# Kernel tuning notes

Hardware: AMD Instinct MI355X
Metric: run time of the kernel (lower is better)

The kernel has to match this reference:

```python
import jax, jax.numpy as jnp
import numpy as np

N = 50000   # nodes
E = 800000  # edges
IN, HID, OUT = 128, 128, 64


def setup_inputs() -> dict:
    key = jax.random.key(0)
    ks = jax.random.split(key, 16)
    x = jax.random.normal(ks[0], (N, IN), dtype=jnp.float32)
    src = jax.random.randint(ks[1], (E,), 0, N, dtype=jnp.int32)
    dst = jax.random.randint(ks[2], (E,), 0, N, dtype=jnp.int32)
    s = 1.0 / np.sqrt(IN)
    W_self1 = jax.random.normal(ks[3], (IN, HID), dtype=jnp.float32) * s
    W_neigh1 = jax.random.normal(ks[4], (IN, HID), dtype=jnp.float32) * s
    b1 = jnp.zeros((HID,), dtype=jnp.float32)
    W_self2 = jax.random.normal(ks[5], (HID, HID), dtype=jnp.float32) * s
    W_neigh2 = jax.random.normal(ks[6], (HID, HID), dtype=jnp.float32) * s
    b2 = jnp.zeros((HID,), dtype=jnp.float32)
    W_self3 = jax.random.normal(ks[7], (HID, OUT), dtype=jnp.float32) * s
    W_neigh3 = jax.random.normal(ks[8], (HID, OUT), dtype=jnp.float32) * s
    b3 = jnp.zeros((OUT,), dtype=jnp.float32)
    # dropout(p=0.5) masks, pre-scaled by 1/(1-p)
    keep = 0.5
    mask1 = (jax.random.uniform(ks[9], (N, HID)) < keep).astype(jnp.float32) / keep
    mask2 = (jax.random.uniform(ks[10], (N, HID)) < keep).astype(jnp.float32) / keep
    return dict(x=x, src=src, dst=dst,
                W_self1=W_self1, W_neigh1=W_neigh1, b1=b1,
                W_self2=W_self2, W_neigh2=W_neigh2, b2=b2,
                W_self3=W_self3, W_neigh3=W_neigh3, b3=b3,
                mask1=mask1, mask2=mask2)


def _mean_agg(h, src, dst):
    # gather source features, segment-sum into destinations, divide by in-degree
    summed = jax.ops.segment_sum(h[src], dst, num_segments=N)  # [N, d]
    deg = jax.ops.segment_sum(jnp.ones((E,), dtype=h.dtype), dst, num_segments=N)
    return summed / jnp.maximum(deg, 1.0)[:, None]


def _sage_layer(h, src, dst, W_self, W_neigh, b):
    h_neigh = _mean_agg(h, src, dst)
    return h @ W_self + h_neigh @ W_neigh + b


def reference(x, src, dst, W_self1, W_neigh1, b1, W_self2, W_neigh2, b2,
              W_self3, W_neigh3, b3, mask1, mask2):
    h = _sage_layer(x, src, dst, W_self1, W_neigh1, b1)
    h = jax.nn.relu(h) * mask1
    h = _sage_layer(h, src, dst, W_self2, W_neigh2, b2)
    h = jax.nn.relu(h) * mask2
    h = _sage_layer(h, src, dst, W_self3, W_neigh3, b3)
    return h
```

## Files before the change

### kernel.cpp

```cpp
#include <hip/hip_runtime.h>
#include <hip/hip_bf16.h>

#define DIN  128
#define DHID 128
#define DOUT 64

#define EB   4096
#define CAPB 5120

typedef short short8 __attribute__((ext_vector_type(8)));
typedef float f32x4  __attribute__((ext_vector_type(4)));

__device__ __forceinline__ ushort f2bf(float f) {
    union { float f; uint u; } c; c.f = f;
    uint u = c.u;
    return (ushort)((u + 0x7fff + ((u >> 16) & 1)) >> 16);
}
__device__ __forceinline__ float bf2f(uint h16) {
    union { uint u; float f; } c; c.u = h16 << 16;
    return c.f;
}
__device__ __forceinline__ float sb8(uint u, int k) {
    return (float)((int)(u << (24 - 8 * k)) >> 24);
}

__device__ __forceinline__ void wprep_dev(const float* __restrict__ W,
                                          ushort* __restrict__ Wt, int OUT, int idx) {
    int nn = idx >> 7;
    int k  = idx & 127;
    Wt[idx] = f2bf(W[(size_t)k * OUT + nn]);
}

__global__ __launch_bounds__(256)
void megaprep(const int* __restrict__ src, const int* __restrict__ dst, int E, int fillB,
              int* __restrict__ bkt_cur, uint* __restrict__ pairs,
              const float* __restrict__ x, ushort* __restrict__ xb, int n4, int cvtB,
              const float* __restrict__ Ws1, const float* __restrict__ Wn1,
              const float* __restrict__ Ws2, const float* __restrict__ Wn2,
              const float* __restrict__ Ws3, const float* __restrict__ Wn3,
              ushort* __restrict__ Wst1, ushort* __restrict__ Wnt1,
              ushort* __restrict__ Wst2, ushort* __restrict__ Wnt2,
              ushort* __restrict__ Wst3, ushort* __restrict__ Wnt3) {
    __shared__ int c[256];
    __shared__ int startl[256];
    __shared__ int ofs[256];
    int b = blockIdx.x;
    const int t = threadIdx.x;
    if (b < fillB) {
        c[t] = 0;
        __syncthreads();
        const int base = b * EB;
        const int end = min(base + EB, E);
        for (int i = base + t; i < end; i += 256)
            atomicAdd(&c[dst[i] >> 8], 1);
        __syncthreads();
        int v = c[t];
        startl[t] = v ? (t * CAPB + atomicAdd(&bkt_cur[t], v)) : 0;
        ofs[t] = 0;
        __syncthreads();
        for (int i = base + t; i < end; i += 256) {
            int d = dst[i];
            int bb = d >> 8;
            int p = startl[bb] + atomicAdd(&ofs[bb], 1);
            pairs[p] = ((uint)src[i] << 8) | (uint)(d & 255);
        }
        return;
    }
    b -= fillB;
    if (b < cvtB) {
        int i = b * 256 + t;
        if (i < n4) {
            float4 v = ((const float4*)x)[i];
            ushort4 o;
            o.x = f2bf(v.x); o.y = f2bf(v.y); o.z = f2bf(v.z); o.w = f2bf(v.w);
            ((ushort4*)xb)[i] = o;
        }
        return;
    }
    b -= cvtB;
    if (b < 64)  { wprep_dev(Ws1, Wst1, 128, b * 256 + t); return; }
    b -= 64;
    if (b < 64)  { wprep_dev(Wn1, Wnt1, 128, b * 256 + t); return; }
    b -= 64;
    if (b < 64)  { wprep_dev(Ws2, Wst2, 128, b * 256 + t); return; }
    b -= 64;
    if (b < 64)  { wprep_dev(Wn2, Wnt2, 128, b * 256 + t); return; }
    b -= 64;
    if (b < 32)  { wprep_dev(Ws3, Wst3, 64, b * 256 + t); return; }
    b -= 32;
    wprep_dev(Wn3, Wnt3, 64, b * 256 + t);
}

__global__ __launch_bounds__(256)
void bucket_csr(const uint* __restrict__ pairs, const int* __restrict__ bkt_cur,
                int* __restrict__ row_ptr, int* __restrict__ deg,
                int* __restrict__ esrc, int N, int nbkt) {
    constexpr int CAP = 6144;
    __shared__ uint pl[CAP];
    __shared__ int cnt[256];
    __shared__ int rs[256];
    __shared__ int sc[256];
    const int bkt = blockIdx.x;
    const int t = threadIdx.x;
    const int ebase = bkt * CAPB;
    const int ecnt  = min(bkt_cur[bkt], CAPB);
    cnt[t] = 0;
    __syncthreads();
    const bool fits = (ecnt <= CAP);
    if (fits) {
        for (int i = t; i < ecnt; i += 256) {
            uint p = pairs[ebase + i];
            pl[i] = p;
            atomicAdd(&cnt[p & 255u], 1);
        }
    } else {
        for (int i = t; i < ecnt; i += 256)
            atomicAdd(&cnt[pairs[ebase + i] & 255u], 1);
    }
    __syncthreads();
    int own = cnt[t];
    sc[t] = own;
    __syncthreads();
    for (int o = 1; o < 256; o <<= 1) {
        int u = (t >= o) ? sc[t - o] : 0;
        __syncthreads();
        sc[t] += u;
        __syncthreads();
    }
    rs[t] = sc[t] - own;
    const int node = bkt * 256 + t;
    if (node < N) {
        row_ptr[node] = ebase + rs[t];
        deg[node] = own;
    }
    __syncthreads();
    if (fits) {
        for (int i = t; i < ecnt; i += 256) {
            uint p = pl[i];
            int pos = atomicAdd(&rs[p & 255u], 1);
            esrc[ebase + pos] = (int)(p >> 8);
        }
    } else {
        for (int i = t; i < ecnt; i += 256) {
            uint p = pairs[ebase + i];
            int pos = atomicAdd(&rs[p & 255u], 1);
            esrc[ebase + pos] = (int)(p >> 8);
        }
    }
}

template<int OUTW>
__global__ __launch_bounds__(256)
void sage_gemm(const ushort* __restrict__ Hb,
               const ushort* __restrict__ Wst,
               const ushort* __restrict__ Wnt,
               ushort* __restrict__ S,
               signed char* __restrict__ Gq,
               float* __restrict__ Gsc,
               int n) {
    constexpr int NT = OUTW / 16;
    __shared__ ushort Wl[2][OUTW * 128];

    const int tid  = threadIdx.x;
    const int lane = tid & 63;
    const int wave = tid >> 6;
    const int rg   = wave >> 1;
    const int isG  = wave & 1;
    const int m16  = lane & 15;
    const int kb   = lane >> 4;
    const int rbase = blockIdx.x * 64 + rg * 32;

    {
        const uint4* s4 = (const uint4*)Wst;
        const uint4* n4 = (const uint4*)Wnt;
        uint4* ls = (uint4*)&Wl[0][0];
        uint4* ln = (uint4*)&Wl[1][0];
#pragma unroll
        for (int j = tid; j < OUTW * 128 / 8; j += 256) {
            ls[j] = s4[j];
            ln[j] = n4[j];
        }
    }

    short8 a[2][4];
#pragma unroll
    for (int mt = 0; mt < 2; ++mt) {
        int arow = rbase + mt * 16 + m16;
        if (arow >= n) arow = n - 1;
        const ushort* __restrict__ Ap = &Hb[(size_t)arow * 128 + kb * 8];
#pragma unroll
        for (int c = 0; c < 4; ++c)
            a[mt][c] = *(const short8*)(Ap + c * 32);
    }

    __syncthreads();

    f32x4 acc[2][NT];
#pragma unroll
    for (int mt = 0; mt < 2; ++mt)
#pragma unroll
        for (int t = 0; t < NT; ++t) acc[mt][t] = (f32x4)(0.f);

    const ushort* __restrict__ Wp = &Wl[isG][0];
#pragma unroll
    for (int t = 0; t < NT; ++t) {
#pragma unroll
        for (int c = 0; c < 4; ++c) {
            short8 b = *(const short8*)&Wp[(t * 16 + m16) * 128 + c * 32 + kb * 8];
            acc[0][t] = __builtin_amdgcn_mfma_f32_16x16x32_bf16(a[0][c], b, acc[0][t], 0, 0, 0);
            acc[1][t] = __builtin_amdgcn_mfma_f32_16x16x32_bf16(a[1][c], b, acc[1][t], 0, 0, 0);
        }
    }

#pragma unroll
    for (int mt = 0; mt < 2; ++mt) {
        const int rb = rbase + mt * 16;
        if (!isG) {
#pragma unroll
            for (int r = 0; r < 4; ++r) {
                int row = rb + kb * 4 + r;
                if (row >= n) continue;
#pragma unroll
                for (int t = 0; t < NT; ++t)
                    S[(size_t)row * OUTW + t * 16 + m16] = f2bf(acc[mt][t][r]);
            }
        } else {
#pragma unroll
            for (int r = 0; r < 4; ++r) {
                float mx = 0.f;
#pragma unroll
                for (int t = 0; t < NT; ++t) mx = fmaxf(mx, fabsf(acc[mt][t][r]));
                mx = fmaxf(mx, __shfl_xor(mx, 1));
                mx = fmaxf(mx, __shfl_xor(mx, 2));
                mx = fmaxf(mx, __shfl_xor(mx, 4));
                mx = fmaxf(mx, __shfl_xor(mx, 8));
                int row = rb + kb * 4 + r;
                if (row >= n) continue;
                float inv = (mx > 0.f) ? 127.f / mx : 0.f;
                if (m16 == 0) Gsc[row] = mx * (1.f / 127.f);
#pragma unroll
                for (int t = 0; t < NT; ++t) {
                    int q = (int)rintf(acc[mt][t][r] * inv);
                    q = max(-127, min(127, q));
                    Gq[(size_t)row * OUTW + t * 16 + m16] = (signed char)q;
                }
            }
        }
    }
}

__device__ __forceinline__ void acc8(float* af, uint2 v, float sc) {
    af[0] += sc * sb8(v.x, 0); af[1] += sc * sb8(v.x, 1);
    af[2] += sc * sb8(v.x, 2); af[3] += sc * sb8(v.x, 3);
    af[4] += sc * sb8(v.y, 0); af[5] += sc * sb8(v.y, 1);
    af[6] += sc * sb8(v.y, 2); af[7] += sc * sb8(v.y, 3);
}
__device__ __forceinline__ void acc16(float* af, uint4 v, float sc) {
    af[0]  += sc * sb8(v.x, 0); af[1]  += sc * sb8(v.x, 1);
    af[2]  += sc * sb8(v.x, 2); af[3]  += sc * sb8(v.x, 3);
    af[4]  += sc * sb8(v.y, 0); af[5]  += sc * sb8(v.y, 1);
    af[6]  += sc * sb8(v.y, 2); af[7]  += sc * sb8(v.y, 3);
    af[8]  += sc * sb8(v.z, 0); af[9]  += sc * sb8(v.z, 1);
    af[10] += sc * sb8(v.z, 2); af[11] += sc * sb8(v.z, 3);
    af[12] += sc * sb8(v.w, 0); af[13] += sc * sb8(v.w, 1);
    af[14] += sc * sb8(v.w, 2); af[15] += sc * sb8(v.w, 3);
}

#define SPAN_CAP 1024

template<bool FINAL>
__global__ __launch_bounds__(256)
void sage_gather(const signed char* __restrict__ Gq, const float* __restrict__ Gsc,
                 const ushort* __restrict__ S, const float* __restrict__ bias,
                 const float* __restrict__ mask,
                 const int* __restrict__ row_ptr, const int* __restrict__ deg,
                 const int* __restrict__ esrc,
                 void* __restrict__ outv, int n) {
    __shared__ int   idx_s[SPAN_CAP];
    __shared__ float sc_s[SPAN_CAP];

    const int tid  = threadIdx.x;
    const int lane = tid & 63;
    const int wave = tid >> 6;
    const int g    = lane >> 3;
    const int l8   = lane & 7;
    const int base = blockIdx.x * 32;

    const int last   = min(base + 31, n - 1);
    const int span_s = row_ptr[base];
    const int span_e = row_ptr[last] + deg[last];
    const int len    = span_e - span_s;
    const bool staged = (len <= SPAN_CAP);
    if (staged) {
        int sA[4];
#pragma unroll
        for (int r = 0; r < 4; ++r) {
            int i = tid + r * 256;
            sA[r] = (i < len) ? esrc[span_s + i] : 0;
        }
#pragma unroll
        for (int r = 0; r < 4; ++r) {
            int i = tid + r * 256;
            if (i < len) { idx_s[i] = sA[r]; sc_s[i] = Gsc[sA[r]]; }
        }
    }
    __syncthreads();

    const int node = base + wave * 8 + g;
    if (node >= n) return;
    const int d = deg[node];
    const float inv = 1.f / fmaxf((float)d, 1.f);

    if (!FINAL) {
        float af[16];
#pragma unroll
        for (int q = 0; q < 16; ++q) af[q] = 0.f;
        const signed char* __restrict__ gp = Gq + l8 * 16;
        if (staged) {
            int i = row_ptr[node] - span_s, e = i + d;
            for (; i + 7 < e; i += 8) {
                uint4 v[8]; float c[8];
#pragma unroll
                for (int k = 0; k < 8; ++k) {
                    int ns = idx_s[i + k];
                    v[k] = *(const uint4*)&gp[(size_t)ns * 128];
                    c[k] = sc_s[i + k];
                }
#pragma unroll
                for (int k = 0; k < 8; ++k) acc16(af, v[k], c[k]);
            }
            for (; i < e; ++i) {
                int ns = idx_s[i];
                acc16(af, *(const uint4*)&gp[(size_t)ns * 128], sc_s[i]);
            }
        } else {
            int i = row_ptr[node], e = i + d;
            for (; i < e; ++i) {
                int ns = esrc[i];
                acc16(af, *(const uint4*)&gp[(size_t)ns * 128], Gsc[ns]);
            }
        }
        const int col0 = l8 * 16;
        uint4 sa = *(const uint4*)&S[(size_t)node * 128 + col0];
        uint4 sb = *(const uint4*)&S[(size_t)node * 128 + col0 + 8];
        float bv[16], mv[16];
#pragma unroll
        for (int q = 0; q < 4; ++q) {
            *(float4*)&bv[q * 4] = *(const float4*)&bias[col0 + q * 4];
            *(float4*)&mv[q * 4] = *(const float4*)&mask[(size_t)node * 128 + col0 + q * 4];
        }
        uint sv[8] = {sa.x, sa.y, sa.z, sa.w, sb.x, sb.y, sb.z, sb.w};
        uint pk[8];
#pragma unroll
        for (int q = 0; q < 8; ++q) {
            float z0 = bf2f(sv[q] & 0xffffu) + af[2 * q]     * inv + bv[2 * q];
            float z1 = bf2f(sv[q] >> 16)     + af[2 * q + 1] * inv + bv[2 * q + 1];
            z0 = fmaxf(z0, 0.f) * mv[2 * q];
            z1 = fmaxf(z1, 0.f) * mv[2 * q + 1];
            pk[q] = (uint)f2bf(z0) | ((uint)f2bf(z1) << 16);
        }
        ushort* op = (ushort*)outv + (size_t)node * 128 + col0;
        uint4 o0, o1;
        o0.x = pk[0]; o0.y = pk[1]; o0.z = pk[2]; o0.w = pk[3];
        o1.x = pk[4]; o1.y = pk[5]; o1.z = pk[6]; o1.w = pk[7];
        *(uint4*)op = o0;
        *(uint4*)(op + 8) = o1;
    } else {
        float af[8];
#pragma unroll
        for (int q = 0; q < 8; ++q) af[q] = 0.f;
        const signed char* __restrict__ gp = Gq + l8 * 8;
        if (staged) {
            int i = row_ptr[node] - span_s, e = i + d;
            for (; i + 7 < e; i += 8) {
                uint2 v[8]; float c[8];
#pragma unroll
                for (int k = 0; k < 8; ++k) {
                    int ns = idx_s[i + k];
                    v[k] = *(const uint2*)&gp[(size_t)ns * 64];
                    c[k] = sc_s[i + k];
                }
#pragma unroll
                for (int k = 0; k < 8; ++k) acc8(af, v[k], c[k]);
            }
            for (; i < e; ++i) {
                int ns = idx_s[i];
                acc8(af, *(const uint2*)&gp[(size_t)ns * 64], sc_s[i]);
            }
        } else {
            int i = row_ptr[node], e = i + d;
            for (; i < e; ++i) {
                int ns = esrc[i];
                acc8(af, *(const uint2*)&gp[(size_t)ns * 64], Gsc[ns]);
            }
        }
        const int col0 = l8 * 8;
        uint4 sv4 = *(const uint4*)&S[(size_t)node * 64 + col0];
        float bv[8];
        *(float4*)&bv[0] = *(const float4*)&bias[col0];
        *(float4*)&bv[4] = *(const float4*)&bias[col0 + 4];
        uint sv[4] = {sv4.x, sv4.y, sv4.z, sv4.w};
        float z[8];
#pragma unroll
        for (int q = 0; q < 4; ++q) {
            z[2 * q]     = bf2f(sv[q] & 0xffffu) + af[2 * q]     * inv + bv[2 * q];
            z[2 * q + 1] = bf2f(sv[q] >> 16)     + af[2 * q + 1] * inv + bv[2 * q + 1];
        }
        float* op = (float*)outv + (size_t)node * 64 + col0;
        float4 o0, o1;
        o0.x = z[0]; o0.y = z[1]; o0.z = z[2]; o0.w = z[3];
        o1.x = z[4]; o1.y = z[5]; o1.z = z[6]; o1.w = z[7];
        *(float4*)&op[0] = o0;
        *(float4*)&op[4] = o1;
    }
}

extern "C" void kernel_launch(void* const* d_in, const int* in_sizes, int n_in,
                              void* d_out, int out_size, void* d_ws, size_t ws_size,
                              hipStream_t stream) {
    const float* x   = (const float*)d_in[0];
    const int*   src = (const int*)d_in[1];
    const int*   dst = (const int*)d_in[2];
    const float* Ws1 = (const float*)d_in[3];
    const float* Wn1 = (const float*)d_in[4];
    const float* b1  = (const float*)d_in[5];
    const float* Ws2 = (const float*)d_in[6];
    const float* Wn2 = (const float*)d_in[7];
    const float* b2  = (const float*)d_in[8];
    const float* Ws3 = (const float*)d_in[9];
    const float* Wn3 = (const float*)d_in[10];
    const float* b3  = (const float*)d_in[11];
    const float* mask1 = (const float*)d_in[12];
    const float* mask2 = (const float*)d_in[13];
    float* out = (float*)d_out;

    const int N = in_sizes[0] / DIN;
    const int E = in_sizes[1];
    const int nbkt = (N + 255) >> 8;

    char* ws = (char*)d_ws;
    int* bkt_cur  = (int*)ws;
    int* row_ptr  = bkt_cur + 256;
    int* deg      = row_ptr + N;
    int* esrc     = deg + N;
    size_t off = ((size_t)(256 + 2 * N + nbkt * CAPB) * sizeof(int) + 255) & ~(size_t)255;
    uint* pairs  = (uint*)(ws + off);    off += (size_t)nbkt * CAPB * 4;
    ushort* xb   = (ushort*)(ws + off);  off += (size_t)N * 128 * 2;
    ushort* h1b  = (ushort*)(ws + off);  off += (size_t)N * 128 * 2;
    ushort* h2b  = (ushort*)(ws + off);  off += (size_t)N * 128 * 2;
    ushort* S    = (ushort*)(ws + off);  off += (size_t)N * 128 * 2;
    signed char* Gq = (signed char*)(ws + off); off += (size_t)N * 128;
    float* Gsc   = (float*)(ws + off);   off += (size_t)N * 4;
    ushort* Wst1 = (ushort*)(ws + off);  off += 128 * 128 * 2;
    ushort* Wnt1 = (ushort*)(ws + off);  off += 128 * 128 * 2;
    ushort* Wst2 = (ushort*)(ws + off);  off += 128 * 128 * 2;
    ushort* Wnt2 = (ushort*)(ws + off);  off += 128 * 128 * 2;
    ushort* Wst3 = (ushort*)(ws + off);  off += 64 * 128 * 2;
    ushort* Wnt3 = (ushort*)(ws + off);  off += 64 * 128 * 2;

    const int n4 = N * 128 / 4;
    const int cvtB = (n4 + 255) / 256;
    const int fillB = (E + EB - 1) / EB;

    hipMemsetAsync(bkt_cur, 0, 256 * sizeof(int), stream);
    megaprep<<<fillB + cvtB + 4 * 64 + 2 * 32, 256, 0, stream>>>(
        src, dst, E, fillB, bkt_cur, pairs,
        x, xb, n4, cvtB,
        Ws1, Wn1, Ws2, Wn2, Ws3, Wn3,
        Wst1, Wnt1, Wst2, Wnt2, Wst3, Wnt3);

    bucket_csr<<<nbkt, 256, 0, stream>>>(pairs, bkt_cur, row_ptr, deg, esrc, N, nbkt);

    const int gemmB = (N + 63) / 64;
    const int gathB = (N + 31) / 32;

    sage_gemm<128><<<gemmB, 256, 0, stream>>>(xb, Wst1, Wnt1, S, Gq, Gsc, N);
    sage_gather<false><<<gathB, 256, 0, stream>>>(Gq, Gsc, S, b1, mask1, row_ptr, deg, esrc, h1b, N);
    sage_gemm<128><<<gemmB, 256, 0, stream>>>(h1b, Wst2, Wnt2, S, Gq, Gsc, N);
    sage_gather<false><<<gathB, 256, 0, stream>>>(Gq, Gsc, S, b2, mask2, row_ptr, deg, esrc, h2b, N);
    sage_gemm<64><<<gemmB, 256, 0, stream>>>(h2b, Wst3, Wnt3, S, Gq, Gsc, N);
    sage_gather<true><<<gathB, 256, 0, stream>>>(Gq, Gsc, S, b3, nullptr, row_ptr, deg, esrc, out, N);
}
```

Before: 291.3 us.

## Stage gather indices per wave and double-buffer neighbor loads in sage_gather

Each wave now stages the edge span for its own 8 nodes into a private LDS slice. Source index and scale are packed together as a uint2, so the block-wide __syncthreads and the two separate LDS arrays go away. Blocks shrink to 128 threads, and the fixed 8-wide gather loop becomes a two-buffer software pipeline of 4-edge groups, so the next group's loads are issued while the current one accumulates. The aim is to remove block-level sync stalls and overlap gather latency with compute. In exchange it adds more code paths and relies on in-wave LDS ordering without an explicit barrier.

New measurement: 284.3 us. -2.4%, faster.

```diff
diff --git a/kernel.cpp b/kernel.cpp
--- a/kernel.cpp
+++ b/kernel.cpp
@@ -266,49 +266,71 @@
     af[14] += sc * sb8(v.w, 2); af[15] += sc * sb8(v.w, 3);
 }
 
-#define SPAN_CAP 1024
+#define WCAP 320
+
+#define LOADW16(V, C, base_)                                        \
+    _Pragma("unroll")                                               \
+    for (int k = 0; k < 4; ++k) {                                   \
+        uint2 p = iw[(base_) + k];                                  \
+        V[k] = *(const uint4*)&gp[(size_t)p.x * 128];               \
+        C[k] = __uint_as_float(p.y);                                \
+    }
+#define LOADW8(V, C, base_)                                         \
+    _Pragma("unroll")                                               \
+    for (int k = 0; k < 4; ++k) {                                   \
+        uint2 p = iw[(base_) + k];                                  \
+        V[k] = *(const uint2*)&gp[(size_t)p.x * 64];                \
+        C[k] = __uint_as_float(p.y);                                \
+    }
+#define CONSW16(V, C)                                               \
+    _Pragma("unroll") for (int k = 0; k < 4; ++k) acc16(af, V[k], C[k]);
+#define CONSW8(V, C)                                                \
+    _Pragma("unroll") for (int k = 0; k < 4; ++k) acc8(af, V[k], C[k]);
 
 template<bool FINAL>
-__global__ __launch_bounds__(256)
+__global__ __launch_bounds__(128)
 void sage_gather(const signed char* __restrict__ Gq, const float* __restrict__ Gsc,
                  const ushort* __restrict__ S, const float* __restrict__ bias,
                  const float* __restrict__ mask,
                  const int* __restrict__ row_ptr, const int* __restrict__ deg,
                  const int* __restrict__ esrc,
                  void* __restrict__ outv, int n) {
-    __shared__ int   idx_s[SPAN_CAP];
-    __shared__ float sc_s[SPAN_CAP];
+    __shared__ uint2 is_s[2][WCAP];
 
     const int tid  = threadIdx.x;
+    const int wave = tid >> 6;
     const int lane = tid & 63;
-    const int wave = tid >> 6;
     const int g    = lane >> 3;
     const int l8   = lane & 7;
-    const int base = blockIdx.x * 32;
-
-    const int last   = min(base + 31, n - 1);
-    const int span_s = row_ptr[base];
+    const int wbase = blockIdx.x * 16 + wave * 8;
+    if (wbase >= n) return;
+
+    const int node = wbase + g;
+    int d = 0, rp = 0;
+    if (node < n) { d = deg[node]; rp = row_ptr[node]; }
+
+    const int last   = min(wbase + 7, n - 1);
+    const int span_s = row_ptr[wbase];
     const int span_e = row_ptr[last] + deg[last];
     const int len    = span_e - span_s;
-    const bool staged = (len <= SPAN_CAP);
+    uint2* __restrict__ iw = is_s[wave];
+    const bool staged = (len <= WCAP);
     if (staged) {
-        int sA[4];
-#pragma unroll
-        for (int r = 0; r < 4; ++r) {
-            int i = tid + r * 256;
+        int sA[5];
+#pragma unroll
+        for (int r = 0; r < 5; ++r) {
+            int i = lane + r * 64;
             sA[r] = (i < len) ? esrc[span_s + i] : 0;
         }
 #pragma unroll
-        for (int r = 0; r < 4; ++r) {
-            int i = tid + r * 256;
-            if (i < len) { idx_s[i] = sA[r]; sc_s[i] = Gsc[sA[r]]; }
-        }
-    }
-    __syncthreads();
-
-    const int node = base + wave * 8 + g;
+        for (int r = 0; r < 5; ++r) {
+            int i = lane + r * 64;
+            if (i < len)
+                iw[i] = make_uint2((uint)sA[r], __float_as_uint(Gsc[sA[r]]));
+        }
+    }
+
     if (node >= n) return;
-    const int d = deg[node];
     const float inv = 1.f / fmaxf((float)d, 1.f);
 
     if (!FINAL) {
@@ -316,31 +338,35 @@
 #pragma unroll
         for (int q = 0; q < 16; ++q) af[q] = 0.f;
         const signed char* __restrict__ gp = Gq + l8 * 16;
+        const int col0 = l8 * 16;
+
         if (staged) {
-            int i = row_ptr[node] - span_s, e = i + d;
-            for (; i + 7 < e; i += 8) {
-                uint4 v[8]; float c[8];
-#pragma unroll
-                for (int k = 0; k < 8; ++k) {
-                    int ns = idx_s[i + k];
-                    v[k] = *(const uint4*)&gp[(size_t)ns * 128];
-                    c[k] = sc_s[i + k];
-                }
-#pragma unroll
-                for (int k = 0; k < 8; ++k) acc16(af, v[k], c[k]);
-            }
+            int i = rp - span_s;
+            const int e = i + d;
+            const int nf = d >> 2;
+            uint4 vA[4], vB[4]; float cA[4], cB[4];
+            if (nf >= 1) { LOADW16(vA, cA, i); }
+            if (nf >= 2) { LOADW16(vB, cB, i + 4); }
+            int b = 0;
+            for (; b + 2 <= nf; b += 2) {
+                CONSW16(vA, cA);
+                if (b + 2 < nf) { LOADW16(vA, cA, i + 8); }
+                CONSW16(vB, cB);
+                if (b + 3 < nf) { LOADW16(vB, cB, i + 12); }
+                i += 8;
+            }
+            if (b < nf) { CONSW16(vA, cA); i += 4; }
             for (; i < e; ++i) {
-                int ns = idx_s[i];
-                acc16(af, *(const uint4*)&gp[(size_t)ns * 128], sc_s[i]);
+                uint2 p = iw[i];
+                acc16(af, *(const uint4*)&gp[(size_t)p.x * 128], __uint_as_float(p.y));
             }
         } else {
-            int i = row_ptr[node], e = i + d;
+            int i = rp, e = i + d;
             for (; i < e; ++i) {
                 int ns = esrc[i];
                 acc16(af, *(const uint4*)&gp[(size_t)ns * 128], Gsc[ns]);
             }
         }
-        const int col0 = l8 * 16;
         uint4 sa = *(const uint4*)&S[(size_t)node * 128 + col0];
         uint4 sb = *(const uint4*)&S[(size_t)node * 128 + col0 + 8];
         float bv[16], mv[16];
@@ -370,31 +396,35 @@
 #pragma unroll
         for (int q = 0; q < 8; ++q) af[q] = 0.f;
         const signed char* __restrict__ gp = Gq + l8 * 8;
+        const int col0 = l8 * 8;
+
         if (staged) {
-            int i = row_ptr[node] - span_s, e = i + d;
-            for (; i + 7 < e; i += 8) {
-                uint2 v[8]; float c[8];
-#pragma unroll
-                for (int k = 0; k < 8; ++k) {
-                    int ns = idx_s[i + k];
-                    v[k] = *(const uint2*)&gp[(size_t)ns * 64];
-                    c[k] = sc_s[i + k];
-                }
-#pragma unroll
-                for (int k = 0; k < 8; ++k) acc8(af, v[k], c[k]);
-            }
+            int i = rp - span_s;
+            const int e = i + d;
+            const int nf = d >> 2;
+            uint2 vA[4], vB[4]; float cA[4], cB[4];
+            if (nf >= 1) { LOADW8(vA, cA, i); }
+            if (nf >= 2) { LOADW8(vB, cB, i + 4); }
+            int b = 0;
+            for (; b + 2 <= nf; b += 2) {
+                CONSW8(vA, cA);
+                if (b + 2 < nf) { LOADW8(vA, cA, i + 8); }
+                CONSW8(vB, cB);
+                if (b + 3 < nf) { LOADW8(vB, cB, i + 12); }
+                i += 8;
+            }
+            if (b < nf) { CONSW8(vA, cA); i += 4; }
             for (; i < e; ++i) {
-                int ns = idx_s[i];
-                acc8(af, *(const uint2*)&gp[(size_t)ns * 64], sc_s[i]);
+                uint2 p = iw[i];
+                acc8(af, *(const uint2*)&gp[(size_t)p.x * 64], __uint_as_float(p.y));
             }
         } else {
-            int i = row_ptr[node], e = i + d;
+            int i = rp, e = i + d;
             for (; i < e; ++i) {
                 int ns = esrc[i];
                 acc8(af, *(const uint2*)&gp[(size_t)ns * 64], Gsc[ns]);
             }
         }
-        const int col0 = l8 * 8;
         uint4 sv4 = *(const uint4*)&S[(size_t)node * 64 + col0];
         float bv[8];
         *(float4*)&bv[0] = *(const float4*)&bias[col0];
@@ -472,12 +502,12 @@
     bucket_csr<<<nbkt, 256, 0, stream>>>(pairs, bkt_cur, row_ptr, deg, esrc, N, nbkt);
 
     const int gemmB = (N + 63) / 64;
-    const int gathB = (N + 31) / 32;
+    const int gathB = (N + 15) / 16;
 
     sage_gemm<128><<<gemmB, 256, 0, stream>>>(xb, Wst1, Wnt1, S, Gq, Gsc, N);
-    sage_gather<false><<<gathB, 256, 0, stream>>>(Gq, Gsc, S, b1, mask1, row_ptr, deg, esrc, h1b, N);
+    sage_gather<false><<<gathB, 128, 0, stream>>>(Gq, Gsc, S, b1, mask1, row_ptr, deg, esrc, h1b, N);
     sage_gemm<128><<<gemmB, 256, 0, stream>>>(h1b, Wst2, Wnt2, S, Gq, Gsc, N);
-    sage_gather<false><<<gathB, 256, 0, stream>>>(Gq, Gsc, S, b2, mask2, row_ptr, deg, esrc, h2b, N);
+    sage_gather<false><<<gathB, 128, 0, stream>>>(Gq, Gsc, S, b2, mask2, row_ptr, deg, esrc, h2b, N);
     sage_gemm<64><<<gemmB, 256, 0, stream>>>(h2b, Wst3, Wnt3, S, Gq, Gsc, N);
-    sage_gather<true><<<gathB, 256, 0, stream>>>(Gq, Gsc, S, b3, nullptr, row_ptr, deg, esrc, out, N);
-}
+    sage_gather<true><<<gathB, 128, 0, stream>>>(Gq, Gsc, S, b3, nullptr, row_ptr, deg, esrc, out, N);
+}
```
